# Kernel optimization log

Hardware: AMD Instinct MI355X
Metric: run time of the kernel (lower is better)

The kernel has to match this reference:

```python
import jax, jax.numpy as jnp
import numpy as np

EMBED_DIM = 1024
NUM_HEADS = 16
HEAD_DIM = EMBED_DIM // NUM_HEADS


def setup_inputs() -> dict:
    key = jax.random.key(0)
    k_x, k_wqkv, k_bqkv, k_wp, k_bp = jax.random.split(key, 5)
    B, S, D = 2, 2048, EMBED_DIM
    bound_qkv = 1.0 / np.sqrt(D)
    bound_p = 1.0 / np.sqrt(D)
    return {
        "x": jax.random.normal(k_x, (B, S, D), dtype=jnp.float32),
        # torch nn.Linear stores weight as (out, in); keep that layout
        "w_qkv": jax.random.uniform(k_wqkv, (3 * D, D), jnp.float32, -bound_qkv, bound_qkv),
        "b_qkv": jax.random.uniform(k_bqkv, (3 * D,), jnp.float32, -bound_qkv, bound_qkv),
        "w_proj": jax.random.uniform(k_wp, (D, D), jnp.float32, -bound_p, bound_p),
        "b_proj": jax.random.uniform(k_bp, (D,), jnp.float32, -bound_p, bound_p),
    }


def reference(x, w_qkv, b_qkv, w_proj, b_proj):
    B, S, D = x.shape
    H, hd = NUM_HEADS, HEAD_DIM
    qkv = x @ w_qkv.T + b_qkv                      # [B,S,3D]
    qkv = qkv.reshape(B, S, 3, H, hd)
    qkv = jnp.transpose(qkv, (2, 0, 3, 1, 4))       # [3,B,H,S,hd]
    q, k, v = qkv[0], qkv[1], qkv[2]
    scale = 1.0 / np.sqrt(hd)
    scores = jnp.einsum('bhqd,bhkd->bhqk', q, k) * scale  # [B,H,S,S]
    attn = jax.nn.softmax(scores, axis=-1)
    out = jnp.einsum('bhqk,bhkd->bhqd', attn, v)    # [B,H,S,hd]
    out = jnp.transpose(out, (0, 2, 1, 3)).reshape(B, S, D)
    return out @ w_proj.T + b_proj
```

## Files before the change

### kernel.cpp

```cpp
#include <hip/hip_runtime.h>
#include <hip/hip_bf16.h>
#include <math.h>


typedef __bf16 bf16_t;
typedef __bf16 bf16x8 __attribute__((ext_vector_type(8)));
typedef __bf16 bf16x4v __attribute__((ext_vector_type(4)));
typedef float f32x4 __attribute__((ext_vector_type(4)));
typedef float f32x16 __attribute__((ext_vector_type(16)));

#define B_ 2
#define S_ 2048
#define D_ 1024
#define H_ 16
#define HD_ 64
#define QSCALE 0.18033688011112042f

__device__ __forceinline__ void load_lds16(const void* g, void* s) {
  __builtin_amdgcn_global_load_lds((__attribute__((address_space(1))) unsigned int*)g,
                                   (__attribute__((address_space(3))) unsigned int*)s,
                                   16, 0, 0);
}

__global__ void tobf16_all(const float* __restrict__ x, const float* __restrict__ wq,
                           const float* __restrict__ wp, bf16_t* __restrict__ xb,
                           bf16_t* __restrict__ wqb, bf16_t* __restrict__ wpb) {
  int bid = blockIdx.x;
  const float* in;
  bf16_t* out;
  int base;
  if (bid < 4096) { in = x; out = xb; base = bid; }
  else if (bid < 7168) { in = wq; out = wqb; base = bid - 4096; }
  else { in = wp; out = wpb; base = bid - 7168; }
  int i = base * 256 + threadIdx.x;
  float4 v = ((const float4*)in)[i];
  bf16x4v o;
  o[0] = (bf16_t)v.x; o[1] = (bf16_t)v.y; o[2] = (bf16_t)v.z; o[3] = (bf16_t)v.w;
  ((bf16x4v*)out)[i] = o;
}

template <int EPI, int BN>
__global__ __launch_bounds__(256, 2) void gemm_bt(
    const bf16_t* __restrict__ A, const bf16_t* __restrict__ Bm,
    const float* __restrict__ bias,
    bf16_t* __restrict__ qb, bf16_t* __restrict__ kb, bf16_t* __restrict__ vtb,
    float* __restrict__ outf) {
  constexpr int NI = BN / 32;
  constexpr int BUF = 8192 + BN * 64;
  __shared__ __align__(16) char smem[2 * BUF];
  const int tid = threadIdx.x;
  const int w = tid >> 6, lane = tid & 63;
  const int wm = w >> 1, wn = w & 1;
  const int quad = lane >> 4, l15 = lane & 15;
  const int m0 = blockIdx.y * 128, n0 = blockIdx.x * BN;

  auto stage = [&](int kt, int bb) {
    char* bA = smem + bb * BUF;
    char* bB = bA + 8192;
#pragma unroll
    for (int i = 0; i < 2; i++) {
      int ub = w * 128 + i * 64;
      int u = ub + lane;
      int r = u >> 2, c = (u & 3) ^ ((r >> 1) & 3);
      load_lds16(A + (size_t)(m0 + r) * 1024 + kt + c * 8, bA + (size_t)ub * 16);
    }
#pragma unroll
    for (int i = 0; i < BN / 64; i++) {
      int ub = w * (BN / 64) * 64 + i * 64;
      int u = ub + lane;
      int r = u >> 2, c = (u & 3) ^ ((r >> 1) & 3);
      load_lds16(Bm + (size_t)(n0 + r) * 1024 + kt + c * 8, bB + (size_t)ub * 16);
    }
  };

  f32x4 acc[4][NI];
#pragma unroll
  for (int mi = 0; mi < 4; mi++)
#pragma unroll
    for (int ni = 0; ni < NI; ni++) acc[mi][ni] = (f32x4){0.f, 0.f, 0.f, 0.f};

  stage(0, 0);

  for (int it = 0; it < 32; it++) {
    __syncthreads();
    if (it < 31) stage((it + 1) * 32, (it + 1) & 1);
    const bf16_t* bA = (const bf16_t*)(smem + (it & 1) * BUF);
    const bf16_t* bB = (const bf16_t*)(smem + (it & 1) * BUF + 8192);

    bf16x8 af[4], bfr[NI];
#pragma unroll
    for (int mi = 0; mi < 4; mi++) {
      int r = wm * 64 + mi * 16 + l15;
      af[mi] = *(const bf16x8*)(bA + (r * 4 + (quad ^ ((r >> 1) & 3))) * 8);
    }
#pragma unroll
    for (int ni = 0; ni < NI; ni++) {
      int r = wn * (BN / 2) + ni * 16 + l15;
      bfr[ni] = *(const bf16x8*)(bB + (r * 4 + (quad ^ ((r >> 1) & 3))) * 8);
    }
#pragma unroll
    for (int mi = 0; mi < 4; mi++)
#pragma unroll
      for (int ni = 0; ni < NI; ni++)
        acc[mi][ni] = __builtin_amdgcn_mfma_f32_16x16x32_bf16(af[mi], bfr[ni], acc[mi][ni], 0, 0, 0);
  }

#pragma unroll
  for (int mi = 0; mi < 4; mi++) {
#pragma unroll
    for (int ni = 0; ni < NI; ni++) {
      int n = n0 + wn * (BN / 2) + ni * 16 + l15;
      float bv = bias[n];
#pragma unroll
      for (int r = 0; r < 4; r++) {
        int m = m0 + wm * 64 + mi * 16 + quad * 4 + r;
        float v = acc[mi][ni][r] + bv;
        if (EPI == 0) {
          int t = n >> 10;
          int rr = n & 1023;
          int hh = rr >> 6, d = rr & 63;
          int bb = m >> 11, s = m & 2047;
          size_t bh = (size_t)(bb * H_ + hh);
          if (t == 0)
            qb[(bh * S_ + s) * HD_ + d] = (bf16_t)(v * QSCALE);
          else if (t == 1)
            kb[(bh * S_ + s) * HD_ + d] = (bf16_t)v;
          else
            vtb[(bh * HD_ + d) * S_ + s] = (bf16_t)v;
        } else {
          outf[(size_t)m * 1024 + n] = v;
        }
      }
    }
  }
}

__global__ __launch_bounds__(256, 2) void attn(
    const bf16_t* __restrict__ qb, const bf16_t* __restrict__ kb,
    const bf16_t* __restrict__ vtb, bf16_t* __restrict__ ob) {
  __shared__ __align__(16) char smem[49152];
  const int tid = threadIdx.x, w = tid >> 6, lane = tid & 63;
  const int h2 = lane >> 5, l31 = lane & 31;
  const int gid = blockIdx.x;
  const int g = gid & 7, k_ = gid >> 3;
  const int bh = g * 4 + (k_ >> 4);
  const int qt = k_ & 15;
  const int b = bh >> 4, h = bh & 15;
  const size_t base = (size_t)bh * S_ * HD_;
  const size_t vbase = (size_t)bh * HD_ * S_;
  const int q0 = qt * 128;
  char* Pw = smem + 32768 + w * 4096;

  bf16x8 aq[4];
#pragma unroll
  for (int ks = 0; ks < 4; ks++)
    aq[ks] = *(const bf16x8*)(qb + base + (size_t)(q0 + w * 32 + l31) * 64 + ks * 16 + h2 * 8);

  auto stage = [&](int kv0, int bb) {
    char* bK = smem + bb * 16384;
    char* bV = bK + 8192;
#pragma unroll
    for (int i = 0; i < 2; i++) {
      int ub = i * 256 + w * 64;
      int u = ub + lane;
      int rk = u >> 3, ck = (u & 7) ^ (rk & 7);
      load_lds16(kb + base + (size_t)(kv0 + rk) * 64 + ck * 8, bK + (size_t)ub * 16);
      int rv = u >> 3, cv = (u & 7) ^ (rv & 7);
      load_lds16(vtb + vbase + (size_t)rv * S_ + kv0 + cv * 8, bV + (size_t)ub * 16);
    }
  };

  f32x16 acc_o[2];
#pragma unroll
  for (int dt = 0; dt < 2; dt++)
#pragma unroll
    for (int i = 0; i < 16; i++) acc_o[dt][i] = 0.f;
  float l_part[16];
#pragma unroll
  for (int i = 0; i < 16; i++) l_part[i] = 0.f;

  stage(0, 0);

  for (int j = 0; j < 32; j++) {
    __syncthreads();
    if (j < 31) stage((j + 1) * 64, (j + 1) & 1);
    const bf16_t* bK = (const bf16_t*)(smem + (j & 1) * 16384);
    const bf16_t* bV = bK + 4096;

    f32x16 s_acc[2];
#pragma unroll
    for (int nt = 0; nt < 2; nt++)
#pragma unroll
      for (int i = 0; i < 16; i++) s_acc[nt][i] = 0.f;
#pragma unroll
    for (int ks = 0; ks < 4; ks++) {
#pragma unroll
      for (int nt = 0; nt < 2; nt++) {
        int r = nt * 32 + l31;
        bf16x8 bk = *(const bf16x8*)(bK + (r * 8 + ((ks * 2 + h2) ^ (r & 7))) * 8);
        s_acc[nt] = __builtin_amdgcn_mfma_f32_32x32x16_bf16(aq[ks], bk, s_acc[nt], 0, 0, 0);
      }
    }

#pragma unroll
    for (int reg = 0; reg < 16; reg++) {
      int rr = (reg & 3) + 8 * (reg >> 2) + 4 * h2;
      float p0 = exp2f(s_acc[0][reg]);
      float p1 = exp2f(s_acc[1][reg]);
      l_part[reg] += p0 + p1;
      int u0 = ((l31 >> 3) ^ (rr & 7));
      int u1 = (((l31 >> 3) + 4) ^ (rr & 7));
      *(bf16_t*)(Pw + rr * 128 + u0 * 16 + (l31 & 7) * 2) = (bf16_t)p0;
      *(bf16_t*)(Pw + rr * 128 + u1 * 16 + (l31 & 7) * 2) = (bf16_t)p1;
    }

#pragma unroll
    for (int ks = 0; ks < 4; ks++) {
      bf16x8 ap = *(const bf16x8*)(Pw + l31 * 128 + (((ks * 2 + h2) ^ (l31 & 7)) * 16));
#pragma unroll
      for (int dt = 0; dt < 2; dt++) {
        int r = dt * 32 + l31;
        bf16x8 bv = *(const bf16x8*)(bV + (r * 8 + ((ks * 2 + h2) ^ (r & 7))) * 8);
        acc_o[dt] = __builtin_amdgcn_mfma_f32_32x32x16_bf16(ap, bv, acc_o[dt], 0, 0, 0);
      }
    }
  }

  float inv_l[16];
#pragma unroll
  for (int reg = 0; reg < 16; reg++) {
    float v = l_part[reg];
    v += __shfl_xor(v, 1);
    v += __shfl_xor(v, 2);
    v += __shfl_xor(v, 4);
    v += __shfl_xor(v, 8);
    v += __shfl_xor(v, 16);
    inv_l[reg] = 1.0f / v;
  }

#pragma unroll
  for (int dt = 0; dt < 2; dt++)
#pragma unroll
    for (int reg = 0; reg < 16; reg++) {
      int rr = (reg & 3) + 8 * (reg >> 2) + 4 * h2;
      int q = q0 + w * 32 + rr;
      int d = dt * 32 + l31;
      float v = acc_o[dt][reg] * inv_l[reg];
      ob[((size_t)b * S_ + q) * D_ + h * HD_ + d] = (bf16_t)v;
    }
}

extern "C" void kernel_launch(void* const* d_in, const int* in_sizes, int n_in,
                              void* d_out, int out_size, void* d_ws, size_t ws_size,
                              hipStream_t stream) {
  const float* x = (const float*)d_in[0];
  const float* w_qkv = (const float*)d_in[1];
  const float* b_qkv = (const float*)d_in[2];
  const float* w_proj = (const float*)d_in[3];
  const float* b_proj = (const float*)d_in[4];
  float* out = (float*)d_out;

  char* ws = (char*)d_ws;
  size_t off = 0;
  bf16_t* xb = (bf16_t*)(ws + off); off += (size_t)4096 * 1024 * 2;
  bf16_t* wqkvb = (bf16_t*)(ws + off); off += (size_t)3072 * 1024 * 2;
  bf16_t* wpb = (bf16_t*)(ws + off); off += (size_t)1024 * 1024 * 2;
  bf16_t* qb = (bf16_t*)(ws + off); off += (size_t)4096 * 1024 * 2;
  bf16_t* kb = (bf16_t*)(ws + off); off += (size_t)4096 * 1024 * 2;
  bf16_t* vtb = (bf16_t*)(ws + off); off += (size_t)4096 * 1024 * 2;
  bf16_t* ob = xb;

  tobf16_all<<<8192, 256, 0, stream>>>(x, w_qkv, w_proj, xb, wqkvb, wpb);
  gemm_bt<0, 128><<<dim3(24, 32), 256, 0, stream>>>(xb, wqkvb, b_qkv, qb, kb, vtb, nullptr);
  attn<<<512, 256, 0, stream>>>(qb, kb, vtb, ob);
  gemm_bt<1, 64><<<dim3(16, 32), 256, 0, stream>>>(ob, wpb, b_proj, nullptr, nullptr, nullptr, out);
}
```

Before: 207.7 us.

## Compute transposed attention scores to keep P in registers, skip LDS round-trip

The attention kernel now computes S^T = K·Q^T so each lane holds scores for its own query column. The exponentiated probabilities are packed to bf16 and swapped across half-waves with shuffles to form the B operand of the PV MFMA, instead of being written to and read back from LDS. The row-sum reduction shrinks to one cross-half shuffle, and output stores become 4-wide vectors. Blocks shrink to 2 waves with 64 queries and LDS drops to 32KB, so the grid doubles. That raises parallelism but halves K/V reuse per block loaded into LDS.

```diff
diff --git a/kernel.cpp b/kernel.cpp
--- a/kernel.cpp
+++ b/kernel.cpp
@@ -6,6 +6,7 @@
 typedef __bf16 bf16_t;
 typedef __bf16 bf16x8 __attribute__((ext_vector_type(8)));
 typedef __bf16 bf16x4v __attribute__((ext_vector_type(4)));
+typedef __bf16 bf16x2 __attribute__((ext_vector_type(2)));
 typedef float f32x4 __attribute__((ext_vector_type(4)));
 typedef float f32x16 __attribute__((ext_vector_type(16)));
 
@@ -20,6 +21,15 @@
   __builtin_amdgcn_global_load_lds((__attribute__((address_space(1))) unsigned int*)g,
                                    (__attribute__((address_space(3))) unsigned int*)s,
                                    16, 0, 0);
+}
+
+__device__ __forceinline__ unsigned pack2(float a, float b) {
+  bf16x2 t;
+  t[0] = (bf16_t)a;
+  t[1] = (bf16_t)b;
+  union { bf16x2 v; unsigned u; } c;
+  c.v = t;
+  return c.u;
 }
 
 __global__ void tobf16_all(const float* __restrict__ x, const float* __restrict__ wq,
@@ -135,38 +145,37 @@
   }
 }
 
-__global__ __launch_bounds__(256, 2) void attn(
+__global__ __launch_bounds__(128, 2) void attn(
     const bf16_t* __restrict__ qb, const bf16_t* __restrict__ kb,
     const bf16_t* __restrict__ vtb, bf16_t* __restrict__ ob) {
-  __shared__ __align__(16) char smem[49152];
+  __shared__ __align__(16) char smem[32768];
   const int tid = threadIdx.x, w = tid >> 6, lane = tid & 63;
   const int h2 = lane >> 5, l31 = lane & 31;
   const int gid = blockIdx.x;
   const int g = gid & 7, k_ = gid >> 3;
-  const int bh = g * 4 + (k_ >> 4);
-  const int qt = k_ & 15;
+  const int bh = g * 4 + (k_ >> 5);
+  const int qt = k_ & 31;
   const int b = bh >> 4, h = bh & 15;
   const size_t base = (size_t)bh * S_ * HD_;
   const size_t vbase = (size_t)bh * HD_ * S_;
-  const int q0 = qt * 128;
-  char* Pw = smem + 32768 + w * 4096;
-
-  bf16x8 aq[4];
+  const int q0 = qt * 64;
+  const int myq = q0 + w * 32 + l31;
+
+  bf16x8 bq[4];
 #pragma unroll
   for (int ks = 0; ks < 4; ks++)
-    aq[ks] = *(const bf16x8*)(qb + base + (size_t)(q0 + w * 32 + l31) * 64 + ks * 16 + h2 * 8);
+    bq[ks] = *(const bf16x8*)(qb + base + (size_t)myq * 64 + ks * 16 + h2 * 8);
 
   auto stage = [&](int kv0, int bb) {
     char* bK = smem + bb * 16384;
     char* bV = bK + 8192;
 #pragma unroll
-    for (int i = 0; i < 2; i++) {
-      int ub = i * 256 + w * 64;
+    for (int i = 0; i < 4; i++) {
+      int ub = w * 256 + i * 64;
       int u = ub + lane;
-      int rk = u >> 3, ck = (u & 7) ^ (rk & 7);
-      load_lds16(kb + base + (size_t)(kv0 + rk) * 64 + ck * 8, bK + (size_t)ub * 16);
-      int rv = u >> 3, cv = (u & 7) ^ (rv & 7);
-      load_lds16(vtb + vbase + (size_t)rv * S_ + kv0 + cv * 8, bV + (size_t)ub * 16);
+      int r = u >> 3, c = (u & 7) ^ (r & 7);
+      load_lds16(kb + base + (size_t)(kv0 + r) * 64 + c * 8, bK + (size_t)ub * 16);
+      load_lds16(vtb + vbase + (size_t)r * S_ + kv0 + c * 8, bV + (size_t)ub * 16);
     }
   };
 
@@ -175,9 +184,7 @@
   for (int dt = 0; dt < 2; dt++)
 #pragma unroll
     for (int i = 0; i < 16; i++) acc_o[dt][i] = 0.f;
-  float l_part[16];
-#pragma unroll
-  for (int i = 0; i < 16; i++) l_part[i] = 0.f;
+  float l_acc = 0.f;
 
   stage(0, 0);
 
@@ -189,64 +196,77 @@
 
     f32x16 s_acc[2];
 #pragma unroll
-    for (int nt = 0; nt < 2; nt++)
-#pragma unroll
-      for (int i = 0; i < 16; i++) s_acc[nt][i] = 0.f;
+    for (int mt = 0; mt < 2; mt++)
+#pragma unroll
+      for (int i = 0; i < 16; i++) s_acc[mt][i] = 0.f;
 #pragma unroll
     for (int ks = 0; ks < 4; ks++) {
 #pragma unroll
-      for (int nt = 0; nt < 2; nt++) {
-        int r = nt * 32 + l31;
-        bf16x8 bk = *(const bf16x8*)(bK + (r * 8 + ((ks * 2 + h2) ^ (r & 7))) * 8);
-        s_acc[nt] = __builtin_amdgcn_mfma_f32_32x32x16_bf16(aq[ks], bk, s_acc[nt], 0, 0, 0);
-      }
-    }
-
-#pragma unroll
-    for (int reg = 0; reg < 16; reg++) {
-      int rr = (reg & 3) + 8 * (reg >> 2) + 4 * h2;
-      float p0 = exp2f(s_acc[0][reg]);
-      float p1 = exp2f(s_acc[1][reg]);
-      l_part[reg] += p0 + p1;
-      int u0 = ((l31 >> 3) ^ (rr & 7));
-      int u1 = (((l31 >> 3) + 4) ^ (rr & 7));
-      *(bf16_t*)(Pw + rr * 128 + u0 * 16 + (l31 & 7) * 2) = (bf16_t)p0;
-      *(bf16_t*)(Pw + rr * 128 + u1 * 16 + (l31 & 7) * 2) = (bf16_t)p1;
-    }
-
-#pragma unroll
-    for (int ks = 0; ks < 4; ks++) {
-      bf16x8 ap = *(const bf16x8*)(Pw + l31 * 128 + (((ks * 2 + h2) ^ (l31 & 7)) * 16));
+      for (int mt = 0; mt < 2; mt++) {
+        int r = mt * 32 + l31, c = ks * 2 + h2;
+        bf16x8 ak = *(const bf16x8*)(bK + (r * 8 + (c ^ (r & 7))) * 8);
+        s_acc[mt] = __builtin_amdgcn_mfma_f32_32x32x16_bf16(ak, bq[ks], s_acc[mt], 0, 0, 0);
+      }
+    }
+
+    bf16x8 av[2][4];
+#pragma unroll
+    for (int ks = 0; ks < 4; ks++)
 #pragma unroll
       for (int dt = 0; dt < 2; dt++) {
-        int r = dt * 32 + l31;
-        bf16x8 bv = *(const bf16x8*)(bV + (r * 8 + ((ks * 2 + h2) ^ (r & 7))) * 8);
-        acc_o[dt] = __builtin_amdgcn_mfma_f32_32x32x16_bf16(ap, bv, acc_o[dt], 0, 0, 0);
-      }
-    }
+        int r = dt * 32 + l31, c = ks * 2 + h2;
+        av[dt][ks] = *(const bf16x8*)(bV + (r * 8 + (c ^ (r & 7))) * 8);
+      }
+
+    unsigned pk[2][8];
+    float ls = 0.f;
+#pragma unroll
+    for (int mt = 0; mt < 2; mt++)
+#pragma unroll
+      for (int i = 0; i < 8; i++) {
+        float p0 = exp2f(s_acc[mt][2 * i]);
+        float p1 = exp2f(s_acc[mt][2 * i + 1]);
+        ls += p0 + p1;
+        pk[mt][i] = pack2(p0, p1);
+      }
+    l_acc += ls;
+
+    bf16x8 bp[4];
+#pragma unroll
+    for (int mt = 0; mt < 2; mt++)
+#pragma unroll
+      for (int kk = 0; kk < 2; kk++) {
+        unsigned a0 = pk[mt][kk * 4 + 0], a1 = pk[mt][kk * 4 + 1];
+        unsigned a2 = pk[mt][kk * 4 + 2], a3 = pk[mt][kk * 4 + 3];
+        unsigned r0 = (unsigned)__shfl_xor((int)(h2 ? a0 : a2), 32);
+        unsigned r1 = (unsigned)__shfl_xor((int)(h2 ? a1 : a3), 32);
+        union { unsigned u[4]; bf16x8 v; } bb;
+        bb.u[0] = h2 ? r0 : a0;
+        bb.u[1] = h2 ? r1 : a1;
+        bb.u[2] = h2 ? a2 : r0;
+        bb.u[3] = h2 ? a3 : r1;
+        bp[mt * 2 + kk] = bb.v;
+      }
+
+#pragma unroll
+    for (int ks = 0; ks < 4; ks++)
+#pragma unroll
+      for (int dt = 0; dt < 2; dt++)
+        acc_o[dt] = __builtin_amdgcn_mfma_f32_32x32x16_bf16(av[dt][ks], bp[ks], acc_o[dt], 0, 0, 0);
   }
 
-  float inv_l[16];
-#pragma unroll
-  for (int reg = 0; reg < 16; reg++) {
-    float v = l_part[reg];
-    v += __shfl_xor(v, 1);
-    v += __shfl_xor(v, 2);
-    v += __shfl_xor(v, 4);
-    v += __shfl_xor(v, 8);
-    v += __shfl_xor(v, 16);
-    inv_l[reg] = 1.0f / v;
-  }
+  float l_tot = l_acc + __shfl_xor(l_acc, 32);
+  float inv = 1.0f / l_tot;
 
 #pragma unroll
   for (int dt = 0; dt < 2; dt++)
 #pragma unroll
-    for (int reg = 0; reg < 16; reg++) {
-      int rr = (reg & 3) + 8 * (reg >> 2) + 4 * h2;
-      int q = q0 + w * 32 + rr;
-      int d = dt * 32 + l31;
-      float v = acc_o[dt][reg] * inv_l[reg];
-      ob[((size_t)b * S_ + q) * D_ + h * HD_ + d] = (bf16_t)v;
+    for (int g4 = 0; g4 < 4; g4++) {
+      bf16x4v o4;
+#pragma unroll
+      for (int i = 0; i < 4; i++) o4[i] = (bf16_t)(acc_o[dt][g4 * 4 + i] * inv);
+      int d = dt * 32 + g4 * 8 + h2 * 4;
+      *(bf16x4v*)(ob + ((size_t)b * S_ + myq) * D_ + h * HD_ + d) = o4;
     }
 }
 
@@ -272,6 +292,6 @@
 
   tobf16_all<<<8192, 256, 0, stream>>>(x, w_qkv, w_proj, xb, wqkvb, wpb);
   gemm_bt<0, 128><<<dim3(24, 32), 256, 0, stream>>>(xb, wqkvb, b_qkv, qb, kb, vtb, nullptr);
-  attn<<<512, 256, 0, stream>>>(qb, kb, vtb, ob);
+  attn<<<1024, 128, 0, stream>>>(qb, kb, vtb, ob);
   gemm_bt<1, 64><<<dim3(16, 32), 256, 0, stream>>>(ob, wpb, b_proj, nullptr, nullptr, nullptr, out);
 }
```

Result: faster. 201.8 us (-2.8%).
